# Kernel optimization log

Hardware: AMD Instinct MI355X
Metric: run time of the kernel (lower is better)

Reference implementation:

```python
import jax, jax.numpy as jnp
import numpy as np

D_MODEL = 1024
NUM_HEADS = 16
HEAD_DIM = D_MODEL // NUM_HEADS


def setup_inputs() -> dict:
    key = jax.random.key(0)
    k_x, k_qkv, k_o = jax.random.split(key, 3)
    B, L = 2, 2048
    x = jax.random.normal(k_x, (B, L, D_MODEL), dtype=jnp.float32)
    # torch Linear weight [out, in]; y = x @ W.T. Scale ~ kaiming-uniform-ish.
    s = 1.0 / np.sqrt(D_MODEL)
    W_qkv = jax.random.uniform(k_qkv, (3 * D_MODEL, D_MODEL), dtype=jnp.float32, minval=-s, maxval=s)
    W_o = jax.random.uniform(k_o, (D_MODEL, D_MODEL), dtype=jnp.float32, minval=-s, maxval=s)
    return {"x": x, "W_qkv": W_qkv, "W_o": W_o}


def reference(x, W_qkv, W_o):
    B, L, D = x.shape
    H, dk = NUM_HEADS, HEAD_DIM
    qkv = (x @ W_qkv.T).reshape(B, L, 3, H, dk)
    q = qkv[:, :, 0].transpose(0, 2, 1, 3)  # [B,H,L,dk]
    k = qkv[:, :, 1].transpose(0, 2, 1, 3)
    v = qkv[:, :, 2].transpose(0, 2, 1, 3)
    scale = 1.0 / np.sqrt(dk).astype(np.float32)
    attn = jnp.einsum('bhqd,bhkd->bhqk', q, k) * scale  # [B,H,L,L]
    causal = jnp.tril(jnp.ones((L, L), dtype=bool))
    attn = jnp.where(causal, attn, -jnp.inf)
    attn = jax.nn.softmax(attn, axis=-1)
    y = jnp.einsum('bhqk,bhkd->bhqd', attn, v)  # [B,H,L,dk]
    y = y.transpose(0, 2, 1, 3).reshape(B, L, D)
    return y @ W_o.T
```

## Files before the change

### kernel.cpp

```cpp
#include <hip/hip_runtime.h>

typedef unsigned short u16;
typedef unsigned int   u32;

typedef __attribute__((ext_vector_type(4))) float  f32x4;
typedef __attribute__((ext_vector_type(8))) __bf16 bf16x8;

#define B_  2
#define L_  2048
#define H_  16

__device__ static inline u16 f2bf(float f) {
  u32 u = __builtin_bit_cast(u32, f);
  u32 r = u + 0x7fffu + ((u >> 16) & 1u);
  return (u16)(r >> 16);
}
__device__ static inline u32 pack2(float a, float b) {
  return (u32)f2bf(a) | ((u32)f2bf(b) << 16);
}
__device__ static inline u32 pack2t(float a, float b) {
  return __builtin_amdgcn_perm(__builtin_bit_cast(u32, b),
                               __builtin_bit_cast(u32, a), 0x07060302u);
}

__device__ static inline void gload_lds16(const u16* g, u16* lds) {
  __builtin_amdgcn_global_load_lds((__attribute__((address_space(1))) void*)(g),
                                   (__attribute__((address_space(3))) void*)(lds),
                                   16, 0, 0);
}

__global__ __launch_bounds__(256) void cvt3_kernel(
    const float4* __restrict__ a, uint2* __restrict__ ao, int na,
    const float4* __restrict__ b, uint2* __restrict__ bo, int nb,
    const float4* __restrict__ c, uint2* __restrict__ co, int nc)
{
  const int step = gridDim.x * 256;
  for (int i = blockIdx.x * 256 + threadIdx.x; i < na; i += step) {
    float4 f = a[i];
    ao[i] = make_uint2(pack2(f.x, f.y), pack2(f.z, f.w));
  }
  for (int i = blockIdx.x * 256 + threadIdx.x; i < nb; i += step) {
    float4 f = b[i];
    bo[i] = make_uint2(pack2(f.x, f.y), pack2(f.z, f.w));
  }
  for (int i = blockIdx.x * 256 + threadIdx.x; i < nc; i += step) {
    float4 f = c[i];
    co[i] = make_uint2(pack2(f.x, f.y), pack2(f.z, f.w));
  }
}

template <bool OUT_F32, int NT, bool DBUF>
__global__ __launch_bounds__(256) void gemm_bt_kernel(
    const u16* __restrict__ A, const u16* __restrict__ Bt, void* __restrict__ Cv,
    const int K, const int N)
{
  constexpr int NB = DBUF ? 2 : 1;
  constexpr int JT = NT / 32;
  __shared__ __attribute__((aligned(16))) u16 Al[NB][128 * 64];
  __shared__ __attribute__((aligned(16))) u16 Bl[NB][NT * 64];

  const int tid  = threadIdx.x;
  const int w    = tid >> 6;
  const int lane = tid & 63;
  const int m0 = blockIdx.y * 128;
  const int n0 = blockIdx.x * NT;
  const int mo = (w >> 1) * 64;
  const int no = (w & 1) * (NT / 2);

  const int sr8  = lane >> 3;
  const int scol = (((lane & 7) ^ ((lane >> 3) & 7)) * 8);

  const f32x4 zero = {0.f, 0.f, 0.f, 0.f};
  f32x4 acc[4][JT];
  #pragma unroll
  for (int i = 0; i < 4; ++i)
    #pragma unroll
    for (int j = 0; j < JT; ++j) acc[i][j] = zero;

  const int frow = lane & 15;
  const int fg   = lane >> 4;

  auto stage = [&](int buf, int k0) {
    #pragma unroll
    for (int inst = 0; inst < 4; ++inst) {
      const int r = w * 32 + inst * 8 + sr8;
      gload_lds16(A + (size_t)(m0 + r) * K + k0 + scol, &Al[buf][(w * 32 + inst * 8) * 64]);
    }
    #pragma unroll
    for (int inst = 0; inst < NT / 32; ++inst) {
      const int r = w * (NT / 4) + inst * 8 + sr8;
      gload_lds16(Bt + (size_t)(n0 + r) * K + k0 + scol, &Bl[buf][(w * (NT / 4) + inst * 8) * 64]);
    }
  };

  if (DBUF) stage(0, 0);

  int cur = 0;
  for (int k0 = 0; k0 < K; k0 += 64) {
    __syncthreads();
    if (DBUF) {
      if (k0 + 64 < K) stage(cur ^ 1, k0 + 64);
    } else {
      stage(0, k0);
      __syncthreads();
    }
    #pragma unroll
    for (int ks = 0; ks < 2; ++ks) {
      const int fco = ((ks * 4 + fg) ^ (frow & 7)) * 8;
      bf16x8 af[4], bfr[JT];
      #pragma unroll
      for (int i = 0; i < 4; ++i)
        af[i] = *(const bf16x8*)&Al[cur][(mo + i * 16 + frow) * 64 + fco];
      #pragma unroll
      for (int j = 0; j < JT; ++j)
        bfr[j] = *(const bf16x8*)&Bl[cur][(no + j * 16 + frow) * 64 + fco];
      #pragma unroll
      for (int i = 0; i < 4; ++i)
        #pragma unroll
        for (int j = 0; j < JT; ++j)
          acc[i][j] = __builtin_amdgcn_mfma_f32_16x16x32_bf16(af[i], bfr[j], acc[i][j], 0, 0, 0);
    }
    if (DBUF) cur ^= 1;
  }

  const int crow0 = m0 + mo + (lane >> 4) * 4;
  const int ccol0 = n0 + no + (lane & 15);
  #pragma unroll
  for (int i = 0; i < 4; ++i)
    #pragma unroll
    for (int j = 0; j < JT; ++j)
      #pragma unroll
      for (int r = 0; r < 4; ++r) {
        const size_t idx = (size_t)(crow0 + i * 16 + r) * N + (ccol0 + j * 16);
        if (OUT_F32) ((float*)Cv)[idx] = acc[i][j][r];
        else         ((u16*)Cv)[idx]   = f2bf(acc[i][j][r]);
      }
}

__global__ __launch_bounds__(512) void attn_mfma_kernel(const u16* __restrict__ qkv,
                                                        u16* __restrict__ y)
{
  __shared__ __attribute__((aligned(16))) unsigned char smem[81920];

  const int tid  = threadIdx.x;
  const int g    = tid >> 8;
  const int w    = (tid >> 6) & 3;
  const int lane = tid & 63;
  const int fr   = lane & 15;
  const int fg   = lane >> 4;
  const int bh   = blockIdx.x;
  const int pi   = blockIdx.y;
  const int bb   = bh >> 4;
  const int hh   = bh & 15;
  const size_t rb = (size_t)bb * L_;

  u16* Kt   = (u16*)(smem + g * 40960);
  u32* Vtd  = (u32*)(smem + g * 40960 + 16384);
  u32* PTd  = (u32*)(smem + g * 40960 + 32768) + w * 512;
  float* Ocmb = (float*)(smem + 40960);
  float* Lcmb = (float*)(smem + 40960 + 17408);

  const int kkp = lane & 31;
  const int dc  = 2 * w + (lane >> 5);

  const int ksr = w * 16 + (lane >> 3);
  const int ksc = (((lane & 7) ^ ((lane >> 3) & 7)) * 8);
  const int kco0 = ((fg) ^ (fr & 7)) * 8;
  const int kco1 = ((4 + fg) ^ (fr & 7)) * 8;

  const int cro0 = 4 * ((fg) ^ (fr & 7));
  const int cro1 = 4 * ((4 + fg) ^ (fr & 7));
  const int pwo  = 4 * (fr & 7);

  const f32x4 zero = {0.f, 0.f, 0.f, 0.f};

  for (int pass = 0; pass < 2; ++pass) {
    const int qt = pass ? (31 - pi) : pi;
    const int q0 = qt * 64;
    const int qw = q0 + w * 16;
    const int n  = qt + 1;
    const int c0 = (n + 1) >> 1;
    const int myCnt  = g ? (n - c0) : c0;
    const int myBase = g ? c0 : 0;
    const int phases = c0;

    const bf16x8 qf0 = *(const bf16x8*)(qkv + (rb + qw + fr) * 3072 + hh * 64 + fg * 8);
    const bf16x8 qf1 = *(const bf16x8*)(qkv + (rb + qw + fr) * 3072 + hh * 64 + 32 + fg * 8);

    f32x4 oacc[4];
    #pragma unroll
    for (int mt = 0; mt < 4; ++mt) oacc[mt] = zero;
    float lsum = 0.f;

    __syncthreads();
    if (myCnt > 0) {
      const int kt = myBase * 64;
      #pragma unroll
      for (int inst = 0; inst < 2; ++inst)
        gload_lds16(qkv + (rb + kt + ksr + inst * 8) * 3072 + 1024 + hh * 64 + ksc,
                    &Kt[(w * 16 + inst * 8) * 64]);
      const u16* vp = qkv + (rb + kt + 2 * kkp) * 3072 + 2048 + hh * 64 + dc * 8;
      uint4 va = *(const uint4*)vp;
      uint4 vb = *(const uint4*)(vp + 3072);
      u16 a16[8], b16[8];
      *(uint4*)a16 = va; *(uint4*)b16 = vb;
      #pragma unroll
      for (int i = 0; i < 8; ++i)
        Vtd[(dc * 8 + i) * 32 + 4 * ((kkp >> 2) ^ i) + (kkp & 3)] =
            (u32)a16[i] | ((u32)b16[i] << 16);
    }

    int cur = 0;
    for (int it = 0; it < phases; ++it) {
      __syncthreads();

      const int  kt       = (myBase + it) * 64;
      const bool active   = it < myCnt;
      const bool havenext = (it + 1) < myCnt;
      uint4 va, vb;
      if (havenext) {
        #pragma unroll
        for (int inst = 0; inst < 2; ++inst)
          gload_lds16(qkv + (rb + kt + 64 + ksr + inst * 8) * 3072 + 1024 + hh * 64 + ksc,
                      &Kt[(cur ^ 1) * 4096 + (w * 16 + inst * 8) * 64]);
        const u16* vp = qkv + (rb + kt + 64 + 2 * kkp) * 3072 + 2048 + hh * 64 + dc * 8;
        va = *(const uint4*)vp;
        vb = *(const uint4*)(vp + 3072);
      }

      if (active) {
        f32x4 sacc[4];
        #pragma unroll
        for (int nt = 0; nt < 4; ++nt) sacc[nt] = zero;
        #pragma unroll
        for (int nt = 0; nt < 4; ++nt) {
          bf16x8 kf0 = *(const bf16x8*)&Kt[cur * 4096 + (nt * 16 + fr) * 64 + kco0];
          sacc[nt] = __builtin_amdgcn_mfma_f32_16x16x32_bf16(kf0, qf0, sacc[nt], 0, 0, 0);
          bf16x8 kf1 = *(const bf16x8*)&Kt[cur * 4096 + (nt * 16 + fr) * 64 + kco1];
          sacc[nt] = __builtin_amdgcn_mfma_f32_16x16x32_bf16(kf1, qf1, sacc[nt], 0, 0, 0);
        }

        if (kt == q0) {
          #pragma unroll
          for (int nt = 0; nt < 4; ++nt) {
            float p[4];
            #pragma unroll
            for (int r = 0; r < 4; ++r) {
              p[r] = (nt * 16 + 4 * fg + r > w * 16 + fr)
                         ? 0.f : __expf(sacc[nt][r] * 0.125f);
              lsum += p[r];
            }
            *(uint2*)&PTd[fr * 32 + ((8 * nt + 2 * fg) ^ pwo)] =
                make_uint2(pack2t(p[0], p[1]), pack2t(p[2], p[3]));
          }
        } else {
          #pragma unroll
          for (int nt = 0; nt < 4; ++nt) {
            float p[4];
            #pragma unroll
            for (int r = 0; r < 4; ++r) {
              p[r] = __expf(sacc[nt][r] * 0.125f);
              lsum += p[r];
            }
            *(uint2*)&PTd[fr * 32 + ((8 * nt + 2 * fg) ^ pwo)] =
                make_uint2(pack2t(p[0], p[1]), pack2t(p[2], p[3]));
          }
        }

        #pragma unroll
        for (int ks = 0; ks < 2; ++ks) {
          bf16x8 pf = *(const bf16x8*)&PTd[fr * 32 + (ks ? cro1 : cro0)];
          #pragma unroll
          for (int mt = 0; mt < 4; ++mt) {
            bf16x8 vf = *(const bf16x8*)&Vtd[cur * 2048 + (mt * 16 + fr) * 32 + (ks ? cro1 : cro0)];
            oacc[mt] = __builtin_amdgcn_mfma_f32_16x16x32_bf16(vf, pf, oacc[mt], 0, 0, 0);
          }
        }
      }

      if (havenext) {
        u16 a16[8], b16[8];
        *(uint4*)a16 = va; *(uint4*)b16 = vb;
        #pragma unroll
        for (int i = 0; i < 8; ++i)
          Vtd[(cur ^ 1) * 2048 + (dc * 8 + i) * 32 + 4 * ((kkp >> 2) ^ i) + (kkp & 3)] =
              (u32)a16[i] | ((u32)b16[i] << 16);
      }
      cur ^= 1;
    }

    lsum += __shfl_xor(lsum, 16);
    lsum += __shfl_xor(lsum, 32);

    __syncthreads();
    if (g == 1) {
      #pragma unroll
      for (int mt = 0; mt < 4; ++mt)
        *(f32x4*)&Ocmb[(w * 16 + fr) * 68 + mt * 16 + 4 * fg] = oacc[mt];
      if (fg == 0) Lcmb[w * 16 + fr] = lsum;
    }
    __syncthreads();
    if (g == 0) {
      const float inv = 1.f / (lsum + Lcmb[w * 16 + fr]);
      u16* yp = y + (rb + qw + fr) * 1024 + hh * 64 + 4 * fg;
      #pragma unroll
      for (int mt = 0; mt < 4; ++mt) {
        f32x4 o = oacc[mt] + *(const f32x4*)&Ocmb[(w * 16 + fr) * 68 + mt * 16 + 4 * fg];
        *(uint2*)(yp + mt * 16) = make_uint2(pack2(o[0] * inv, o[1] * inv),
                                             pack2(o[2] * inv, o[3] * inv));
      }
    }
  }
}

extern "C" void kernel_launch(void* const* d_in, const int* in_sizes, int n_in,
                              void* d_out, int out_size, void* d_ws, size_t ws_size,
                              hipStream_t stream)
{
  const float* x    = (const float*)d_in[0];
  const float* Wqkv = (const float*)d_in[1];
  const float* Wo   = (const float*)d_in[2];
  float* out = (float*)d_out;

  u16* xb    = (u16*)d_ws;
  u16* Wqkvb = xb    + (size_t)4096 * 1024;
  u16* Wob   = Wqkvb + (size_t)3072 * 1024;
  u16* qkv   = Wob   + (size_t)1024 * 1024;
  u16* y     = qkv   + (size_t)4096 * 3072;

  cvt3_kernel<<<dim3(2048), dim3(256), 0, stream>>>(
      (const float4*)x,    (uint2*)xb,    4096 * 1024 / 4,
      (const float4*)Wqkv, (uint2*)Wqkvb, 3072 * 1024 / 4,
      (const float4*)Wo,   (uint2*)Wob,   1024 * 1024 / 4);

  gemm_bt_kernel<false, 128, false><<<dim3(3072 / 128, 4096 / 128), dim3(256), 0, stream>>>(
      xb, Wqkvb, qkv, 1024, 3072);
  attn_mfma_kernel<<<dim3(B_ * H_, 16), dim3(512), 0, stream>>>(qkv, y);
  gemm_bt_kernel<true, 64, true><<<dim3(1024 / 64, 4096 / 128), dim3(256), 0, stream>>>(
      y, Wob, out, 1024, 1024);
}
```

Before: 165.5 us.

## Split attention into one 256-thread block per query tile, fold scale into Wq

The attention kernel drops the two-group 512-thread design, where each block handled two query tiles and split the key range between two thread groups that then merged partial results through shared memory. It now launches one 256-thread block per query tile and orders the tiles so blocks of different lengths are interleaved. This removes the cross-group merge and its barriers and halves LDS per block, but longer tiles now run serially in one block. The 1/sqrt(dk) scale is folded into the Q rows of W_qkv during bf16 conversion, and s_setprio hints are placed around the MFMA sections.

```diff
diff --git a/kernel.cpp b/kernel.cpp
--- a/kernel.cpp
+++ b/kernel.cpp
@@ -35,13 +35,15 @@
     const float4* __restrict__ c, uint2* __restrict__ co, int nc)
 {
   const int step = gridDim.x * 256;
+  constexpr int nq = 1024 * 1024 / 4;
   for (int i = blockIdx.x * 256 + threadIdx.x; i < na; i += step) {
     float4 f = a[i];
     ao[i] = make_uint2(pack2(f.x, f.y), pack2(f.z, f.w));
   }
   for (int i = blockIdx.x * 256 + threadIdx.x; i < nb; i += step) {
     float4 f = b[i];
-    bo[i] = make_uint2(pack2(f.x, f.y), pack2(f.z, f.w));
+    const float s = (i < nq) ? 0.125f : 1.0f;
+    bo[i] = make_uint2(pack2(f.x * s, f.y * s), pack2(f.z * s, f.w * s));
   }
   for (int i = blockIdx.x * 256 + threadIdx.x; i < nc; i += step) {
     float4 f = c[i];
@@ -137,28 +139,28 @@
       }
 }
 
-__global__ __launch_bounds__(512) void attn_mfma_kernel(const u16* __restrict__ qkv,
+__global__ __launch_bounds__(256) void attn_mfma_kernel(const u16* __restrict__ qkv,
                                                         u16* __restrict__ y)
 {
-  __shared__ __attribute__((aligned(16))) unsigned char smem[81920];
+  __shared__ __attribute__((aligned(16))) unsigned char smem[40960];
 
   const int tid  = threadIdx.x;
-  const int g    = tid >> 8;
-  const int w    = (tid >> 6) & 3;
+  const int w    = tid >> 6;
   const int lane = tid & 63;
   const int fr   = lane & 15;
   const int fg   = lane >> 4;
   const int bh   = blockIdx.x;
-  const int pi   = blockIdx.y;
   const int bb   = bh >> 4;
   const int hh   = bh & 15;
   const size_t rb = (size_t)bb * L_;
 
-  u16* Kt   = (u16*)(smem + g * 40960);
-  u32* Vtd  = (u32*)(smem + g * 40960 + 16384);
-  u32* PTd  = (u32*)(smem + g * 40960 + 32768) + w * 512;
-  float* Ocmb = (float*)(smem + 40960);
-  float* Lcmb = (float*)(smem + 40960 + 17408);
+  const int a  = blockIdx.y & 7;
+  const int cc = blockIdx.y >> 3;
+  const int qt = (cc == 0) ? a : (cc == 1) ? (31 - a) : (cc == 2) ? (8 + a) : (23 - a);
+
+  u16* Kt  = (u16*)(smem);
+  u32* Vtd = (u32*)(smem + 16384);
+  u32* PTd = (u32*)(smem + 32768) + w * 512;
 
   const int kkp = lane & 31;
   const int dc  = 2 * w + (lane >> 5);
@@ -174,142 +176,123 @@
 
   const f32x4 zero = {0.f, 0.f, 0.f, 0.f};
 
-  for (int pass = 0; pass < 2; ++pass) {
-    const int qt = pass ? (31 - pi) : pi;
-    const int q0 = qt * 64;
-    const int qw = q0 + w * 16;
-    const int n  = qt + 1;
-    const int c0 = (n + 1) >> 1;
-    const int myCnt  = g ? (n - c0) : c0;
-    const int myBase = g ? c0 : 0;
-    const int phases = c0;
-
-    const bf16x8 qf0 = *(const bf16x8*)(qkv + (rb + qw + fr) * 3072 + hh * 64 + fg * 8);
-    const bf16x8 qf1 = *(const bf16x8*)(qkv + (rb + qw + fr) * 3072 + hh * 64 + 32 + fg * 8);
-
-    f32x4 oacc[4];
-    #pragma unroll
-    for (int mt = 0; mt < 4; ++mt) oacc[mt] = zero;
-    float lsum = 0.f;
-
+  const int q0 = qt * 64;
+  const int qw = q0 + w * 16;
+  const int n  = qt + 1;
+
+  const bf16x8 qf0 = *(const bf16x8*)(qkv + (rb + qw + fr) * 3072 + hh * 64 + fg * 8);
+  const bf16x8 qf1 = *(const bf16x8*)(qkv + (rb + qw + fr) * 3072 + hh * 64 + 32 + fg * 8);
+
+  f32x4 oacc[4];
+  #pragma unroll
+  for (int mt = 0; mt < 4; ++mt) oacc[mt] = zero;
+  float lsum = 0.f;
+
+  {
+    #pragma unroll
+    for (int inst = 0; inst < 2; ++inst)
+      gload_lds16(qkv + (rb + ksr + inst * 8) * 3072 + 1024 + hh * 64 + ksc,
+                  &Kt[(w * 16 + inst * 8) * 64]);
+    const u16* vp = qkv + (rb + 2 * kkp) * 3072 + 2048 + hh * 64 + dc * 8;
+    uint4 va = *(const uint4*)vp;
+    uint4 vb = *(const uint4*)(vp + 3072);
+    u16 a16[8], b16[8];
+    *(uint4*)a16 = va; *(uint4*)b16 = vb;
+    #pragma unroll
+    for (int i = 0; i < 8; ++i)
+      Vtd[(dc * 8 + i) * 32 + 4 * ((kkp >> 2) ^ i) + (kkp & 3)] =
+          (u32)a16[i] | ((u32)b16[i] << 16);
+  }
+
+  int cur = 0;
+  for (int it = 0; it < n; ++it) {
     __syncthreads();
-    if (myCnt > 0) {
-      const int kt = myBase * 64;
+
+    const int  kt       = it * 64;
+    const bool havenext = (it + 1) < n;
+    uint4 va, vb;
+    if (havenext) {
       #pragma unroll
       for (int inst = 0; inst < 2; ++inst)
-        gload_lds16(qkv + (rb + kt + ksr + inst * 8) * 3072 + 1024 + hh * 64 + ksc,
-                    &Kt[(w * 16 + inst * 8) * 64]);
-      const u16* vp = qkv + (rb + kt + 2 * kkp) * 3072 + 2048 + hh * 64 + dc * 8;
-      uint4 va = *(const uint4*)vp;
-      uint4 vb = *(const uint4*)(vp + 3072);
+        gload_lds16(qkv + (rb + kt + 64 + ksr + inst * 8) * 3072 + 1024 + hh * 64 + ksc,
+                    &Kt[(cur ^ 1) * 4096 + (w * 16 + inst * 8) * 64]);
+      const u16* vp = qkv + (rb + kt + 64 + 2 * kkp) * 3072 + 2048 + hh * 64 + dc * 8;
+      va = *(const uint4*)vp;
+      vb = *(const uint4*)(vp + 3072);
+    }
+
+    f32x4 sacc[4];
+    #pragma unroll
+    for (int nt = 0; nt < 4; ++nt) sacc[nt] = zero;
+    __builtin_amdgcn_s_setprio(1);
+    #pragma unroll
+    for (int nt = 0; nt < 4; ++nt) {
+      bf16x8 kf0 = *(const bf16x8*)&Kt[cur * 4096 + (nt * 16 + fr) * 64 + kco0];
+      sacc[nt] = __builtin_amdgcn_mfma_f32_16x16x32_bf16(kf0, qf0, sacc[nt], 0, 0, 0);
+      bf16x8 kf1 = *(const bf16x8*)&Kt[cur * 4096 + (nt * 16 + fr) * 64 + kco1];
+      sacc[nt] = __builtin_amdgcn_mfma_f32_16x16x32_bf16(kf1, qf1, sacc[nt], 0, 0, 0);
+    }
+    __builtin_amdgcn_s_setprio(0);
+
+    if (kt == q0) {
+      #pragma unroll
+      for (int nt = 0; nt < 4; ++nt) {
+        float p[4];
+        #pragma unroll
+        for (int r = 0; r < 4; ++r) {
+          p[r] = (nt * 16 + 4 * fg + r > w * 16 + fr) ? 0.f : __expf(sacc[nt][r]);
+          lsum += p[r];
+        }
+        *(uint2*)&PTd[fr * 32 + ((8 * nt + 2 * fg) ^ pwo)] =
+            make_uint2(pack2t(p[0], p[1]), pack2t(p[2], p[3]));
+      }
+    } else {
+      #pragma unroll
+      for (int nt = 0; nt < 4; ++nt) {
+        float p[4];
+        #pragma unroll
+        for (int r = 0; r < 4; ++r) {
+          p[r] = __expf(sacc[nt][r]);
+          lsum += p[r];
+        }
+        *(uint2*)&PTd[fr * 32 + ((8 * nt + 2 * fg) ^ pwo)] =
+            make_uint2(pack2t(p[0], p[1]), pack2t(p[2], p[3]));
+      }
+    }
+
+    __builtin_amdgcn_s_setprio(1);
+    #pragma unroll
+    for (int ks = 0; ks < 2; ++ks) {
+      bf16x8 pf = *(const bf16x8*)&PTd[fr * 32 + (ks ? cro1 : cro0)];
+      #pragma unroll
+      for (int mt = 0; mt < 4; ++mt) {
+        bf16x8 vf = *(const bf16x8*)&Vtd[cur * 2048 + (mt * 16 + fr) * 32 + (ks ? cro1 : cro0)];
+        oacc[mt] = __builtin_amdgcn_mfma_f32_16x16x32_bf16(vf, pf, oacc[mt], 0, 0, 0);
+      }
+    }
+    __builtin_amdgcn_s_setprio(0);
+
+    if (havenext) {
       u16 a16[8], b16[8];
       *(uint4*)a16 = va; *(uint4*)b16 = vb;
       #pragma unroll
       for (int i = 0; i < 8; ++i)
-        Vtd[(dc * 8 + i) * 32 + 4 * ((kkp >> 2) ^ i) + (kkp & 3)] =
+        Vtd[(cur ^ 1) * 2048 + (dc * 8 + i) * 32 + 4 * ((kkp >> 2) ^ i) + (kkp & 3)] =
             (u32)a16[i] | ((u32)b16[i] << 16);
     }
-
-    int cur = 0;
-    for (int it = 0; it < phases; ++it) {
-      __syncthreads();
-
-      const int  kt       = (myBase + it) * 64;
-      const bool active   = it < myCnt;
-      const bool havenext = (it + 1) < myCnt;
-      uint4 va, vb;
-      if (havenext) {
-        #pragma unroll
-        for (int inst = 0; inst < 2; ++inst)
-          gload_lds16(qkv + (rb + kt + 64 + ksr + inst * 8) * 3072 + 1024 + hh * 64 + ksc,
-                      &Kt[(cur ^ 1) * 4096 + (w * 16 + inst * 8) * 64]);
-        const u16* vp = qkv + (rb + kt + 64 + 2 * kkp) * 3072 + 2048 + hh * 64 + dc * 8;
-        va = *(const uint4*)vp;
-        vb = *(const uint4*)(vp + 3072);
-      }
-
-      if (active) {
-        f32x4 sacc[4];
-        #pragma unroll
-        for (int nt = 0; nt < 4; ++nt) sacc[nt] = zero;
-        #pragma unroll
-        for (int nt = 0; nt < 4; ++nt) {
-          bf16x8 kf0 = *(const bf16x8*)&Kt[cur * 4096 + (nt * 16 + fr) * 64 + kco0];
-          sacc[nt] = __builtin_amdgcn_mfma_f32_16x16x32_bf16(kf0, qf0, sacc[nt], 0, 0, 0);
-          bf16x8 kf1 = *(const bf16x8*)&Kt[cur * 4096 + (nt * 16 + fr) * 64 + kco1];
-          sacc[nt] = __builtin_amdgcn_mfma_f32_16x16x32_bf16(kf1, qf1, sacc[nt], 0, 0, 0);
-        }
-
-        if (kt == q0) {
-          #pragma unroll
-          for (int nt = 0; nt < 4; ++nt) {
-            float p[4];
-            #pragma unroll
-            for (int r = 0; r < 4; ++r) {
-              p[r] = (nt * 16 + 4 * fg + r > w * 16 + fr)
-                         ? 0.f : __expf(sacc[nt][r] * 0.125f);
-              lsum += p[r];
-            }
-            *(uint2*)&PTd[fr * 32 + ((8 * nt + 2 * fg) ^ pwo)] =
-                make_uint2(pack2t(p[0], p[1]), pack2t(p[2], p[3]));
-          }
-        } else {
-          #pragma unroll
-          for (int nt = 0; nt < 4; ++nt) {
-            float p[4];
-            #pragma unroll
-            for (int r = 0; r < 4; ++r) {
-              p[r] = __expf(sacc[nt][r] * 0.125f);
-              lsum += p[r];
-            }
-            *(uint2*)&PTd[fr * 32 + ((8 * nt + 2 * fg) ^ pwo)] =
-                make_uint2(pack2t(p[0], p[1]), pack2t(p[2], p[3]));
-          }
-        }
-
-        #pragma unroll
-        for (int ks = 0; ks < 2; ++ks) {
-          bf16x8 pf = *(const bf16x8*)&PTd[fr * 32 + (ks ? cro1 : cro0)];
-          #pragma unroll
-          for (int mt = 0; mt < 4; ++mt) {
-            bf16x8 vf = *(const bf16x8*)&Vtd[cur * 2048 + (mt * 16 + fr) * 32 + (ks ? cro1 : cro0)];
-            oacc[mt] = __builtin_amdgcn_mfma_f32_16x16x32_bf16(vf, pf, oacc[mt], 0, 0, 0);
-          }
-        }
-      }
-
-      if (havenext) {
-        u16 a16[8], b16[8];
-        *(uint4*)a16 = va; *(uint4*)b16 = vb;
-        #pragma unroll
-        for (int i = 0; i < 8; ++i)
-          Vtd[(cur ^ 1) * 2048 + (dc * 8 + i) * 32 + 4 * ((kkp >> 2) ^ i) + (kkp & 3)] =
-              (u32)a16[i] | ((u32)b16[i] << 16);
-      }
-      cur ^= 1;
-    }
-
-    lsum += __shfl_xor(lsum, 16);
-    lsum += __shfl_xor(lsum, 32);
-
-    __syncthreads();
-    if (g == 1) {
-      #pragma unroll
-      for (int mt = 0; mt < 4; ++mt)
-        *(f32x4*)&Ocmb[(w * 16 + fr) * 68 + mt * 16 + 4 * fg] = oacc[mt];
-      if (fg == 0) Lcmb[w * 16 + fr] = lsum;
-    }
-    __syncthreads();
-    if (g == 0) {
-      const float inv = 1.f / (lsum + Lcmb[w * 16 + fr]);
-      u16* yp = y + (rb + qw + fr) * 1024 + hh * 64 + 4 * fg;
-      #pragma unroll
-      for (int mt = 0; mt < 4; ++mt) {
-        f32x4 o = oacc[mt] + *(const f32x4*)&Ocmb[(w * 16 + fr) * 68 + mt * 16 + 4 * fg];
-        *(uint2*)(yp + mt * 16) = make_uint2(pack2(o[0] * inv, o[1] * inv),
-                                             pack2(o[2] * inv, o[3] * inv));
-      }
-    }
+    cur ^= 1;
+  }
+
+  lsum += __shfl_xor(lsum, 16);
+  lsum += __shfl_xor(lsum, 32);
+  const float inv = 1.f / lsum;
+
+  u16* yp = y + (rb + qw + fr) * 1024 + hh * 64 + 4 * fg;
+  #pragma unroll
+  for (int mt = 0; mt < 4; ++mt) {
+    f32x4 o = oacc[mt];
+    *(uint2*)(yp + mt * 16) = make_uint2(pack2(o[0] * inv, o[1] * inv),
+                                         pack2(o[2] * inv, o[3] * inv));
   }
 }
 
@@ -335,7 +318,7 @@
 
   gemm_bt_kernel<false, 128, false><<<dim3(3072 / 128, 4096 / 128), dim3(256), 0, stream>>>(
       xb, Wqkvb, qkv, 1024, 3072);
-  attn_mfma_kernel<<<dim3(B_ * H_, 16), dim3(512), 0, stream>>>(qkv, y);
+  attn_mfma_kernel<<<dim3(B_ * H_, 32), dim3(256), 0, stream>>>(qkv, y);
   gemm_bt_kernel<true, 64, true><<<dim3(1024 / 64, 4096 / 128), dim3(256), 0, stream>>>(
       y, Wob, out, 1024, 1024);
 }
```

Result: slower. 169.3 us (+2.3%).
